# Performance work log

Hardware: AMD Instinct MI355X
Metric: run time of the kernel (lower is better)

The kernel has to match this reference:

```python
import jax, jax.numpy as jnp
import numpy as np

B, L, E, H = 2, 2048, 1024, 16
A = E // H

def setup_inputs() -> dict:
    key = jax.random.key(0)
    k1, k2, k3, k4 = jax.random.split(key, 4)
    embeddings = jax.random.normal(k1, (B, L, E), dtype=jnp.float32)
    weights = jax.random.normal(k2, (B, H, L, L), dtype=jnp.float32)
    # strictly-upper-triangular True entries mask out future positions
    causal_mask = jnp.triu(jnp.ones((L, L), dtype=bool), k=1)[None, None, :, :]
    V_w = jax.random.normal(k3, (E, E), dtype=jnp.float32) / np.sqrt(E)
    out_w = jax.random.normal(k4, (E, E), dtype=jnp.float32) / np.sqrt(E)
    return {"embeddings": embeddings, "weights": weights,
            "causal_mask": causal_mask, "V_w": V_w, "out_w": out_w}

def reference(embeddings, weights, causal_mask, V_w, out_w):
    # v = Linear(E,E,bias=False): x @ W.T, then split heads -> [B,H,L,A]
    v = jnp.einsum('ble,fe->blf', embeddings, V_w)
    v = v.reshape(B, L, H, A).transpose(0, 2, 1, 3)
    neg = jnp.finfo(weights.dtype).min
    w = jnp.where(causal_mask, neg, weights)
    w = jax.nn.softmax(w, axis=-1)                       # [B,H,L,L]
    values = jnp.einsum('bhqk,bhka->bhqa', w, v)         # [B,H,L,A]
    values = values.transpose(0, 2, 1, 3).reshape(B, L, E)
    return jnp.einsum('ble,fe->blf', values, out_w)
```

## Files before the change

### kernel.cpp

```cpp
#include <hip/hip_runtime.h>

#define TB 2
#define TL 2048
#define TE 1024
#define TH 16
#define TA 64

typedef __bf16 bf16;
typedef __bf16 bf16x4 __attribute__((ext_vector_type(4)));
typedef __bf16 bf16x8 __attribute__((ext_vector_type(8)));
typedef float f32x4 __attribute__((ext_vector_type(4)));

#define AS1 __attribute__((address_space(1)))
#define AS3 __attribute__((address_space(3)))

__device__ __forceinline__ void gload_lds16(const void* g, void* l) {
    __builtin_amdgcn_global_load_lds((const AS1 void*)g, (AS3 void*)l, 16, 0, 0);
}

__global__ __launch_bounds__(256)
void cvt_bf16(const float* __restrict__ in, bf16* __restrict__ out, int n4) {
    int i = blockIdx.x * 256 + threadIdx.x;
    if (i < n4) {
        float4 v = reinterpret_cast<const float4*>(in)[i];
        bf16x4 o = { (bf16)v.x, (bf16)v.y, (bf16)v.z, (bf16)v.w };
        reinterpret_cast<bf16x4*>(out)[i] = o;
    }
}

template<int OUT_MODE>
__global__ __launch_bounds__(256)
void gemm_bt(const bf16* __restrict__ A, const bf16* __restrict__ W, void* Cp) {
    __shared__ __align__(16) bf16 As[128 * 32];
    __shared__ __align__(16) bf16 Bs[128 * 32];
    const int t = threadIdx.x, l = t & 63, w = t >> 6;
    const int m0 = blockIdx.y * 128, n0 = blockIdx.x * 128;
    const int wm = w >> 1, wn = w & 1;

    f32x4 acc[4][4] = {};

    const int rowS = t >> 2;
    const int kbyt = (t & 3) * 16;
    const char* Ag0 = (const char*)(A + (size_t)(m0 + rowS) * 1024) + kbyt;
    const char* Bg0 = (const char*)(W + (size_t)(n0 + rowS) * 1024) + kbyt;
    const int ROWB = 64 * 1024 * 2;
    char* AsB = (char*)As + w * 1024;
    char* BsB = (char*)Bs + w * 1024;

    for (int k0 = 0; k0 < 1024; k0 += 32) {
        const int kB = k0 * 2;
        gload_lds16(Ag0 + kB, AsB);
        gload_lds16(Ag0 + kB + ROWB, AsB + 4096);
        gload_lds16(Bg0 + kB, BsB);
        gload_lds16(Bg0 + kB + ROWB, BsB + 4096);
        __syncthreads();

        bf16x8 af[4], bfr[4];
        #pragma unroll
        for (int mf = 0; mf < 4; ++mf)
            af[mf] = *reinterpret_cast<const bf16x8*>(
                (const char*)As + (wm * 64 + mf * 16 + (l & 15)) * 64 + (l >> 4) * 16);
        #pragma unroll
        for (int nf = 0; nf < 4; ++nf)
            bfr[nf] = *reinterpret_cast<const bf16x8*>(
                (const char*)Bs + (wn * 64 + nf * 16 + (l & 15)) * 64 + (l >> 4) * 16);
        #pragma unroll
        for (int mf = 0; mf < 4; ++mf)
            #pragma unroll
            for (int nf = 0; nf < 4; ++nf)
                acc[mf][nf] = __builtin_amdgcn_mfma_f32_16x16x32_bf16(
                    af[mf], bfr[nf], acc[mf][nf], 0, 0, 0);
        __syncthreads();
    }

    if (OUT_MODE == 0) {
        float* C = (float*)Cp;
        #pragma unroll
        for (int mf = 0; mf < 4; ++mf) {
            const int m = m0 + wm * 64 + mf * 16 + (l >> 4) * 4;
            #pragma unroll
            for (int nf = 0; nf < 4; ++nf) {
                const int n = n0 + wn * 64 + nf * 16 + (l & 15);
                #pragma unroll
                for (int r = 0; r < 4; ++r)
                    C[(size_t)(m + r) * 1024 + n] = acc[mf][nf][r];
            }
        }
    } else {
        bf16* vT = (bf16*)Cp;
        #pragma unroll
        for (int mf = 0; mf < 4; ++mf) {
            const int m = m0 + wm * 64 + mf * 16 + (l >> 4) * 4;
            const int b = m >> 11, lp = m & 2047;
            #pragma unroll
            for (int nf = 0; nf < 4; ++nf) {
                const int n = n0 + wn * 64 + nf * 16 + (l & 15);
                const int h = n >> 6, a = n & 63;
                bf16x4 o = { (bf16)acc[mf][nf][0], (bf16)acc[mf][nf][1],
                             (bf16)acc[mf][nf][2], (bf16)acc[mf][nf][3] };
                *reinterpret_cast<bf16x4*>(
                    &vT[((size_t)(b * TH + h) * TA + a) * TL + lp]) = o;
            }
        }
    }
}

__global__ __launch_bounds__(256)
void attn_mfma(const float* __restrict__ Wt,
               const bf16* __restrict__ vT,
               bf16* __restrict__ Vals) {
    __shared__ __align__(16) char vt[8192];
    const int t = threadIdx.x, l = t & 63, w = t >> 6;
    const int bh = blockIdx.x;
    const int q0 = (31 - (int)blockIdx.y) * 64;
    const int qg = q0 + w * 16 + (l & 15);
    const float* wrow = Wt + (size_t)bh * TL * TL + (size_t)qg * TL;
    const bf16* vTb = vT + (size_t)bh * TA * TL;
    const int kq = (l >> 4) * 8;

    int aR[2], xR[2];
    #pragma unroll
    for (int r = 0; r < 2; ++r) {
        const int o = (t + r * 256) * 16;
        const int a = o >> 7;
        aR[r] = a;
        xR[r] = (o ^ ((a & 7) << 4)) & 127;
    }
    char* ldst = vt + w * 1024;

    f32x4 acc[4] = {};
    float rs = 0.f;
    const int nk = (q0 >> 6) + 1;

    for (int kt = 0; kt < nk; ++kt) {
        const int k0 = kt << 6;
        #pragma unroll
        for (int r = 0; r < 2; ++r)
            gload_lds16((const char*)(vTb + (size_t)aR[r] * TL + k0) + xR[r],
                        ldst + r * 4096);
        bf16x8 pa[2];
        #pragma unroll
        for (int kk = 0; kk < 2; ++kk) {
            const float* wp = wrow + k0 + kk * 32 + kq;
            const float4 x0 = *reinterpret_cast<const float4*>(wp);
            const float4 x1 = *reinterpret_cast<const float4*>(wp + 4);
            const float xs[8] = {x0.x, x0.y, x0.z, x0.w, x1.x, x1.y, x1.z, x1.w};
            #pragma unroll
            for (int j = 0; j < 8; ++j) {
                const int kgl = k0 + kk * 32 + kq + j;
                const float p = (kgl <= qg) ? __expf(xs[j]) : 0.f;
                rs += p;
                pa[kk][j] = (bf16)p;
            }
        }
        __syncthreads();
        #pragma unroll
        for (int nf = 0; nf < 4; ++nf) {
            const int a = nf * 16 + (l & 15);
            const int base = a * 128 + (l >> 4) * 16;
            const int sw = (a & 7) << 4;
            const bf16x8 b0 = *reinterpret_cast<const bf16x8*>(vt + (base ^ sw));
            const bf16x8 b1 = *reinterpret_cast<const bf16x8*>(vt + ((base + 64) ^ sw));
            acc[nf] = __builtin_amdgcn_mfma_f32_16x16x32_bf16(pa[0], b0, acc[nf], 0, 0, 0);
            acc[nf] = __builtin_amdgcn_mfma_f32_16x16x32_bf16(pa[1], b1, acc[nf], 0, 0, 0);
        }
        __syncthreads();
    }

    rs += __shfl_xor(rs, 16);
    rs += __shfl_xor(rs, 32);
    float inv[4];
    #pragma unroll
    for (int r = 0; r < 4; ++r)
        inv[r] = 1.f / __shfl(rs, ((l >> 4) << 2) + r);

    const int b = bh >> 4, h = bh & 15;
    #pragma unroll
    for (int nf = 0; nf < 4; ++nf) {
        const int e = h * 64 + nf * 16 + (l & 15);
        #pragma unroll
        for (int r = 0; r < 4; ++r) {
            const int qq = q0 + w * 16 + (l >> 4) * 4 + r;
            Vals[(size_t)(b * TL + qq) * TE + e] = (bf16)(acc[nf][r] * inv[r]);
        }
    }
}

extern "C" void kernel_launch(void* const* d_in, const int* in_sizes, int n_in,
                              void* d_out, int out_size, void* d_ws, size_t ws_size,
                              hipStream_t stream) {
    const float* emb   = (const float*)d_in[0];
    const float* wts   = (const float*)d_in[1];
    const float* V_w   = (const float*)d_in[3];
    const float* out_w = (const float*)d_in[4];
    float* out = (float*)d_out;

    bf16* embB = (bf16*)d_ws;
    bf16* VwB  = embB + (size_t)4096 * 1024;
    bf16* OwB  = VwB + (size_t)1024 * 1024;
    bf16* vT   = OwB + (size_t)1024 * 1024;
    bf16* vals = vT  + (size_t)4096 * 1024;

    cvt_bf16<<<4096, 256, 0, stream>>>(emb, embB, 1024 * 1024);
    cvt_bf16<<<1024, 256, 0, stream>>>(V_w, VwB, 256 * 1024);
    cvt_bf16<<<1024, 256, 0, stream>>>(out_w, OwB, 256 * 1024);

    dim3 gg(1024 / 128, 4096 / 128);
    gemm_bt<1><<<gg, 256, 0, stream>>>(embB, VwB, (void*)vT);

    dim3 ga(32, 32);
    attn_mfma<<<ga, 256, 0, stream>>>(wts, vT, vals);

    gemm_bt<0><<<gg, 256, 0, stream>>>(vals, OwB, (void*)out);
}
```

Before: 761.7 us.

## Double-buffer GEMM LDS tiles and load V fragments directly in attention

The GEMM kernel now double-buffers its A/B LDS tiles, issuing the next k-step's global-to-LDS loads before computing on the current buffer, which removes one barrier per iteration. The attention kernel drops the shared-memory staging of V and its two block barriers, and instead has each wave read its MFMA B-fragments straight from global memory (L2-cached). This removes barrier stalls in the attention loop, which is bound by streaming the fp32 weights, at the cost of redundant global reads of V across waves and doubled LDS use in the GEMM.

```diff
diff --git a/kernel.cpp b/kernel.cpp
--- a/kernel.cpp
+++ b/kernel.cpp
@@ -31,8 +31,8 @@
 template<int OUT_MODE>
 __global__ __launch_bounds__(256)
 void gemm_bt(const bf16* __restrict__ A, const bf16* __restrict__ W, void* Cp) {
-    __shared__ __align__(16) bf16 As[128 * 32];
-    __shared__ __align__(16) bf16 Bs[128 * 32];
+    __shared__ __align__(16) bf16 As[2][128 * 32];
+    __shared__ __align__(16) bf16 Bs[2][128 * 32];
     const int t = threadIdx.x, l = t & 63, w = t >> 6;
     const int m0 = blockIdx.y * 128, n0 = blockIdx.x * 128;
     const int wm = w >> 1, wn = w & 1;
@@ -44,26 +44,32 @@
     const char* Ag0 = (const char*)(A + (size_t)(m0 + rowS) * 1024) + kbyt;
     const char* Bg0 = (const char*)(W + (size_t)(n0 + rowS) * 1024) + kbyt;
     const int ROWB = 64 * 1024 * 2;
-    char* AsB = (char*)As + w * 1024;
-    char* BsB = (char*)Bs + w * 1024;
-
-    for (int k0 = 0; k0 < 1024; k0 += 32) {
+
+    auto stage = [&](int buf, int k0) {
         const int kB = k0 * 2;
+        char* AsB = (char*)As[buf] + w * 1024;
+        char* BsB = (char*)Bs[buf] + w * 1024;
         gload_lds16(Ag0 + kB, AsB);
         gload_lds16(Ag0 + kB + ROWB, AsB + 4096);
         gload_lds16(Bg0 + kB, BsB);
         gload_lds16(Bg0 + kB + ROWB, BsB + 4096);
-        __syncthreads();
-
+    };
+
+    stage(0, 0);
+    __syncthreads();
+    int cur = 0;
+    #pragma unroll 1
+    for (int step = 0; step < 32; ++step) {
+        if (step + 1 < 32) stage(cur ^ 1, (step + 1) * 32);
         bf16x8 af[4], bfr[4];
         #pragma unroll
         for (int mf = 0; mf < 4; ++mf)
             af[mf] = *reinterpret_cast<const bf16x8*>(
-                (const char*)As + (wm * 64 + mf * 16 + (l & 15)) * 64 + (l >> 4) * 16);
+                (const char*)As[cur] + (wm * 64 + mf * 16 + (l & 15)) * 64 + (l >> 4) * 16);
         #pragma unroll
         for (int nf = 0; nf < 4; ++nf)
             bfr[nf] = *reinterpret_cast<const bf16x8*>(
-                (const char*)Bs + (wn * 64 + nf * 16 + (l & 15)) * 64 + (l >> 4) * 16);
+                (const char*)Bs[cur] + (wn * 64 + nf * 16 + (l & 15)) * 64 + (l >> 4) * 16);
         #pragma unroll
         for (int mf = 0; mf < 4; ++mf)
             #pragma unroll
@@ -71,6 +77,7 @@
                 acc[mf][nf] = __builtin_amdgcn_mfma_f32_16x16x32_bf16(
                     af[mf], bfr[nf], acc[mf][nf], 0, 0, 0);
         __syncthreads();
+        cur ^= 1;
     }
 
     if (OUT_MODE == 0) {
@@ -109,7 +116,6 @@
 void attn_mfma(const float* __restrict__ Wt,
                const bf16* __restrict__ vT,
                bf16* __restrict__ Vals) {
-    __shared__ __align__(16) char vt[8192];
     const int t = threadIdx.x, l = t & 63, w = t >> 6;
     const int bh = blockIdx.x;
     const int q0 = (31 - (int)blockIdx.y) * 64;
@@ -118,26 +124,20 @@
     const bf16* vTb = vT + (size_t)bh * TA * TL;
     const int kq = (l >> 4) * 8;
 
-    int aR[2], xR[2];
-    #pragma unroll
-    for (int r = 0; r < 2; ++r) {
-        const int o = (t + r * 256) * 16;
-        const int a = o >> 7;
-        aR[r] = a;
-        xR[r] = (o ^ ((a & 7) << 4)) & 127;
-    }
-    char* ldst = vt + w * 1024;
-
     f32x4 acc[4] = {};
     float rs = 0.f;
     const int nk = (q0 >> 6) + 1;
 
+    #pragma unroll 1
     for (int kt = 0; kt < nk; ++kt) {
         const int k0 = kt << 6;
-        #pragma unroll
-        for (int r = 0; r < 2; ++r)
-            gload_lds16((const char*)(vTb + (size_t)aR[r] * TL + k0) + xR[r],
-                        ldst + r * 4096);
+        bf16x8 bfr[4][2];
+        #pragma unroll
+        for (int nf = 0; nf < 4; ++nf)
+            #pragma unroll
+            for (int kk = 0; kk < 2; ++kk)
+                bfr[nf][kk] = *reinterpret_cast<const bf16x8*>(
+                    vTb + (size_t)(nf * 16 + (l & 15)) * TL + k0 + kk * 32 + kq);
         bf16x8 pa[2];
         #pragma unroll
         for (int kk = 0; kk < 2; ++kk) {
@@ -153,18 +153,11 @@
                 pa[kk][j] = (bf16)p;
             }
         }
-        __syncthreads();
         #pragma unroll
         for (int nf = 0; nf < 4; ++nf) {
-            const int a = nf * 16 + (l & 15);
-            const int base = a * 128 + (l >> 4) * 16;
-            const int sw = (a & 7) << 4;
-            const bf16x8 b0 = *reinterpret_cast<const bf16x8*>(vt + (base ^ sw));
-            const bf16x8 b1 = *reinterpret_cast<const bf16x8*>(vt + ((base + 64) ^ sw));
-            acc[nf] = __builtin_amdgcn_mfma_f32_16x16x32_bf16(pa[0], b0, acc[nf], 0, 0, 0);
-            acc[nf] = __builtin_amdgcn_mfma_f32_16x16x32_bf16(pa[1], b1, acc[nf], 0, 0, 0);
-        }
-        __syncthreads();
+            acc[nf] = __builtin_amdgcn_mfma_f32_16x16x32_bf16(pa[0], bfr[nf][0], acc[nf], 0, 0, 0);
+            acc[nf] = __builtin_amdgcn_mfma_f32_16x16x32_bf16(pa[1], bfr[nf][1], acc[nf], 0, 0, 0);
+        }
     }
 
     rs += __shfl_xor(rs, 16);
```

Measured after the change: 769.6 us. Within noise of the previous version (+1.0%).
